# Optimization experiments

Hardware: AMD Instinct MI355X
Metric: run time of the kernel (lower is better)

Reference implementation:

```python
import jax, jax.numpy as jnp
import numpy as np

EPS = 1e-10
MARGIN = 0.05
DELTA = 0.1
H = W = 512
N = 8388608


def setup_inputs() -> dict:
    key = jax.random.key(0)
    k1, k2, k3, k4 = jax.random.split(key, 4)
    v_input = jax.random.uniform(k1, (3, H, W), dtype=jnp.float32)
    coords = jax.random.randint(k2, (N, 4), 0, W, dtype=jnp.int32)  # x1,y1,x2,y2
    darker = jax.random.randint(k3, (N,), 0, 3, dtype=jnp.int32)
    weights = jax.random.uniform(k4, (N,), dtype=jnp.float32)
    return {"v_input": v_input, "coords": coords, "darker": darker, "weights": weights}


def reference(v_input, coords, darker, weights):
    # v = sum over channels / 3, then affine remap (exactly as torch code)
    v = jnp.sum(v_input, axis=0) / 3.0
    v = (v * 255.0 + 1.0) / 256.0  # [H, W]

    x1, y1, x2, y2 = coords[:, 0], coords[:, 1], coords[:, 2], coords[:, 3]
    r1 = v[y1, x1]
    r2 = v[y2, x2]
    ratio = r1 / (r2 + EPS)
    ratio_inv = r2 / (r1 + EPS)

    b = 1.0 + DELTA + MARGIN
    inv_b = 1.0 / b
    # darker == 1: penalize if ratio > 1/b
    l1 = jnp.where(ratio > inv_b, (ratio - inv_b) + (b - ratio_inv), 0.0)
    # darker == 2: penalize if ratio < b
    l2 = jnp.where(ratio < b, (b - ratio) + (ratio_inv - inv_b), 0.0)
    # darker == 0 (margin <= delta branch): two-sided hinge around [bl, br]
    br = 1.0 + DELTA - MARGIN
    bl = 1.0 / br
    l0 = jnp.where(
        ratio > br,
        (ratio - br) + (bl - ratio_inv),
        jnp.where(ratio < bl, (bl - ratio) + (ratio_inv - br), 0.0),
    )

    per = jnp.where(darker == 1, l1, jnp.where(darker == 2, l2, l0))
    loss = jnp.sum(weights * per) / np.float32(coords.shape[0])
    return loss
```

## Files before the change

kernel.cpp:

```cpp
#include <hip/hip_runtime.h>

#define HW 512
#define NPIX (HW * HW)
#define LDS_PIX 163840
#define THREADS 1024
#define BLOCKS 512
#define NB 4

#define EPS_F  1e-10f
constexpr double B_d  = 1.0 + 0.1 + 0.05;
constexpr double BR_d = 1.0 + 0.1 - 0.05;
#define B_F    ((float)B_d)
#define INVB_F ((float)(1.0 / B_d))
#define BR_F   ((float)BR_d)
#define BL_F   ((float)(1.0 / BR_d))

typedef __attribute__((ext_vector_type(4))) int ivec4;

__global__ void build_v(const float* __restrict__ vin,
                        unsigned char* __restrict__ vq,
                        float* __restrict__ out) {
    int i = blockIdx.x * blockDim.x + threadIdx.x;
    if (i == 0) *out = 0.0f;
    if (i < NPIX) {
        float s = vin[i] + vin[i + NPIX] + vin[i + 2 * NPIX];
        float m = s * (1.0f / 3.0f);
        vq[i] = (unsigned char)__float2int_rn(m * 255.0f);
    }
}

__device__ __forceinline__ float rcp_fast(float x) {
#if __has_builtin(__builtin_amdgcn_rcpf)
    return __builtin_amdgcn_rcpf(x);
#else
    return 1.0f / x;
#endif
}

__device__ __forceinline__ float per_loss(float r1, float r2, int d) {
    float ratio = r1 * rcp_fast(r2 + EPS_F);
    float rinv  = r2 * rcp_fast(r1 + EPS_F);
    float l1 = (ratio > INVB_F) ? (ratio - INVB_F + (B_F - rinv)) : 0.0f;
    float l2 = (ratio < B_F)    ? (B_F - ratio + (rinv - INVB_F)) : 0.0f;
    float l0 = (ratio > BR_F)   ? (ratio - BR_F + (BL_F - rinv))
             : ((ratio < BL_F)  ? (BL_F - ratio + (rinv - BR_F)) : 0.0f);
    return (d == 1) ? l1 : ((d == 2) ? l2 : l0);
}


__device__ __forceinline__ void load_c(ivec4 (&cc)[NB], const ivec4* __restrict__ coords,
                                       int tid, int T, int ofs) {
    #pragma unroll
    for (int k = 0; k < NB; ++k)
        cc[k] = __builtin_nontemporal_load(&coords[tid + (ofs + k) * T]);
}

__device__ __forceinline__ void load_dw(int (&dd)[NB], float (&ww)[NB],
                                        const int* __restrict__ darker,
                                        const float* __restrict__ weights,
                                        int tid, int T, int ofs) {
    #pragma unroll
    for (int k = 0; k < NB; ++k)
        dd[k] = __builtin_nontemporal_load(&darker[tid + (ofs + k) * T]);
    #pragma unroll
    for (int k = 0; k < NB; ++k)
        ww[k] = __builtin_nontemporal_load(&weights[tid + (ofs + k) * T]);
}

__device__ __forceinline__ void gather_issue(const ivec4 (&cc)[NB],
        unsigned (&q1)[NB], unsigned (&q2)[NB],
        const unsigned char* lv, const unsigned char* __restrict__ vq) {
    #pragma unroll
    for (int k = 0; k < NB; ++k) {
        int i1 = cc[k].y * HW + cc[k].x;
        int i2 = cc[k].w * HW + cc[k].z;
        if (i1 < LDS_PIX) q1[k] = lv[i1]; else q1[k] = vq[i1];
        if (i2 < LDS_PIX) q2[k] = lv[i2]; else q2[k] = vq[i2];
    }
}

__device__ __forceinline__ void consume(const unsigned (&q1)[NB], const unsigned (&q2)[NB],
                                        const int (&dd)[NB], const float (&ww)[NB],
                                        float& acc) {
    #pragma unroll
    for (int k = 0; k < NB; ++k) {
        float r1 = (float)(q1[k] + 1) * (1.0f / 256.0f);
        float r2 = (float)(q2[k] + 1) * (1.0f / 256.0f);
        acc += ww[k] * per_loss(r1, r2, dd[k]);
    }
}

#define SBAR() __builtin_amdgcn_sched_barrier(0)

__global__ __launch_bounds__(THREADS)
__attribute__((amdgpu_waves_per_eu(4, 4)))
void whdr_kernel(
        const unsigned char* __restrict__ vq,
        const ivec4* __restrict__ coords,
        const int*   __restrict__ darker,
        const float* __restrict__ weights,
        float*       __restrict__ out,
        int n) {
    __shared__ unsigned char lv[LDS_PIX];
    const int tid = blockIdx.x * THREADS + threadIdx.x;
    const int T   = BLOCKS * THREADS;
    float acc = 0.0f;

    if (n == T * NB * 4) {
        ivec4 cA[NB], cB[NB];
        int   dA[NB], dB[NB];
        float wA[NB], wB[NB];
        unsigned qa1[NB], qa2[NB], qb1[NB], qb2[NB];

        load_c (cA, coords, tid, T, 0);
        load_dw(dA, wA, darker, weights, tid, T, 0);
        load_c (cB, coords, tid, T, NB);
        load_dw(dB, wB, darker, weights, tid, T, NB);
        {
            const uint4* s4 = (const uint4*)vq;
            uint4* d4 = (uint4*)lv;
            #pragma unroll
            for (int j = threadIdx.x; j < LDS_PIX / 16; j += THREADS) d4[j] = s4[j];
        }
        __syncthreads();

        gather_issue(cA, qa1, qa2, lv, vq);            SBAR();
        gather_issue(cB, qb1, qb2, lv, vq);            SBAR();
        load_c (cA, coords, tid, T, 2 * NB);           SBAR();
        consume(qa1, qa2, dA, wA, acc);
        load_dw(dA, wA, darker, weights, tid, T, 2 * NB); SBAR();
        gather_issue(cA, qa1, qa2, lv, vq);            SBAR();
        load_c (cB, coords, tid, T, 3 * NB);           SBAR();
        consume(qb1, qb2, dB, wB, acc);
        load_dw(dB, wB, darker, weights, tid, T, 3 * NB); SBAR();
        gather_issue(cB, qb1, qb2, lv, vq);            SBAR();
        consume(qa1, qa2, dA, wA, acc);
        consume(qb1, qb2, dB, wB, acc);
    } else {
        {
            const uint4* s4 = (const uint4*)vq;
            uint4* d4 = (uint4*)lv;
            for (int j = threadIdx.x; j < LDS_PIX / 16; j += THREADS) d4[j] = s4[j];
        }
        __syncthreads();
        const int TT = gridDim.x * THREADS;
        for (int i = tid; i < n; i += TT) {
            ivec4 c = coords[i];
            int i1 = c.y * HW + c.x, i2 = c.w * HW + c.z;
            unsigned a = (i1 < LDS_PIX) ? (unsigned)lv[i1] : (unsigned)vq[i1];
            unsigned b = (i2 < LDS_PIX) ? (unsigned)lv[i2] : (unsigned)vq[i2];
            float r1 = (float)(a + 1) * (1.0f / 256.0f);
            float r2 = (float)(b + 1) * (1.0f / 256.0f);
            acc += weights[i] * per_loss(r1, r2, darker[i]);
        }
    }

    #pragma unroll
    for (int off = 32; off > 0; off >>= 1)
        acc += __shfl_down(acc, off, 64);
    __syncthreads();
    float* wsum = (float*)lv;
    int lane = threadIdx.x & 63;
    int wid  = threadIdx.x >> 6;
    if (lane == 0) wsum[wid] = acc;
    __syncthreads();
    if (threadIdx.x == 0) {
        float s = 0.0f;
        #pragma unroll
        for (int i = 0; i < THREADS / 64; ++i) s += wsum[i];
        atomicAdd(out, s / (float)n);
    }
}

extern "C" void kernel_launch(void* const* d_in, const int* in_sizes, int n_in,
                              void* d_out, int out_size, void* d_ws, size_t ws_size,
                              hipStream_t stream) {
    const float* v_input = (const float*)d_in[0];
    const ivec4* coords  = (const ivec4*)d_in[1];
    const int*   darker  = (const int*)d_in[2];
    const float* weights = (const float*)d_in[3];
    float* out = (float*)d_out;
    unsigned char* vq = (unsigned char*)d_ws;
    int n = in_sizes[2];

    build_v<<<(NPIX + 255) / 256, 256, 0, stream>>>(v_input, vq, out);
    whdr_kernel<<<BLOCKS, THREADS, 0, stream>>>(vq, coords, darker, weights, out, n);
}
```

Measured before the change: 246.7 us.

## Drop LDS staging of pixel table and gather directly from global with deeper pipeline

Removes the per-block copy of 160KB of the quantized image into LDS, so every gather now reads the 256KB byte table straight from global memory, where it should stay cache-resident. The launch goes from 512 blocks of 1024 threads to 2048 blocks of 256 threads, with 8 waves per EU and a macro-unrolled 8-round double-buffered pipeline of 2 elements per round. The intent is to cut the redundant per-block staging traffic and the sync, and to raise occupancy. In exchange, every gather becomes a global/L2 byte load instead of an LDS hit, which adds latency.

```diff
diff --git a/kernel.cpp b/kernel.cpp
--- a/kernel.cpp
+++ b/kernel.cpp
@@ -2,10 +2,10 @@
 
 #define HW 512
 #define NPIX (HW * HW)
-#define LDS_PIX 163840
-#define THREADS 1024
-#define BLOCKS 512
-#define NB 4
+#define THREADS 256
+#define BLOCKS 2048
+#define NB 2
+#define RNDS 8
 
 #define EPS_F  1e-10f
 constexpr double B_d  = 1.0 + 0.1 + 0.05;
@@ -69,13 +69,11 @@
 
 __device__ __forceinline__ void gather_issue(const ivec4 (&cc)[NB],
         unsigned (&q1)[NB], unsigned (&q2)[NB],
-        const unsigned char* lv, const unsigned char* __restrict__ vq) {
+        const unsigned char* __restrict__ vq) {
     #pragma unroll
     for (int k = 0; k < NB; ++k) {
-        int i1 = cc[k].y * HW + cc[k].x;
-        int i2 = cc[k].w * HW + cc[k].z;
-        if (i1 < LDS_PIX) q1[k] = lv[i1]; else q1[k] = vq[i1];
-        if (i2 < LDS_PIX) q2[k] = lv[i2]; else q2[k] = vq[i2];
+        q1[k] = vq[cc[k].y * HW + cc[k].x];
+        q2[k] = vq[cc[k].w * HW + cc[k].z];
     }
 }
 
@@ -93,7 +91,7 @@
 #define SBAR() __builtin_amdgcn_sched_barrier(0)
 
 __global__ __launch_bounds__(THREADS)
-__attribute__((amdgpu_waves_per_eu(4, 4)))
+__attribute__((amdgpu_waves_per_eu(8, 8)))
 void whdr_kernel(
         const unsigned char* __restrict__ vq,
         const ivec4* __restrict__ coords,
@@ -101,54 +99,44 @@
         const float* __restrict__ weights,
         float*       __restrict__ out,
         int n) {
-    __shared__ unsigned char lv[LDS_PIX];
     const int tid = blockIdx.x * THREADS + threadIdx.x;
     const int T   = BLOCKS * THREADS;
     float acc = 0.0f;
 
-    if (n == T * NB * 4) {
+    if (n == T * NB * RNDS) {
         ivec4 cA[NB], cB[NB];
         int   dA[NB], dB[NB];
         float wA[NB], wB[NB];
-        unsigned qa1[NB], qa2[NB], qb1[NB], qb2[NB];
+        unsigned qA1[NB], qA2[NB], qB1[NB], qB2[NB];
 
         load_c (cA, coords, tid, T, 0);
         load_dw(dA, wA, darker, weights, tid, T, 0);
         load_c (cB, coords, tid, T, NB);
         load_dw(dB, wB, darker, weights, tid, T, NB);
-        {
-            const uint4* s4 = (const uint4*)vq;
-            uint4* d4 = (uint4*)lv;
-            #pragma unroll
-            for (int j = threadIdx.x; j < LDS_PIX / 16; j += THREADS) d4[j] = s4[j];
-        }
-        __syncthreads();
+        gather_issue(cA, qA1, qA2, vq);                SBAR();
 
-        gather_issue(cA, qa1, qa2, lv, vq);            SBAR();
-        gather_issue(cB, qb1, qb2, lv, vq);            SBAR();
-        load_c (cA, coords, tid, T, 2 * NB);           SBAR();
-        consume(qa1, qa2, dA, wA, acc);
-        load_dw(dA, wA, darker, weights, tid, T, 2 * NB); SBAR();
-        gather_issue(cA, qa1, qa2, lv, vq);            SBAR();
-        load_c (cB, coords, tid, T, 3 * NB);           SBAR();
-        consume(qb1, qb2, dB, wB, acc);
-        load_dw(dB, wB, darker, weights, tid, T, 3 * NB); SBAR();
-        gather_issue(cB, qb1, qb2, lv, vq);            SBAR();
-        consume(qa1, qa2, dA, wA, acc);
-        consume(qb1, qb2, dB, wB, acc);
+#define RPF(r, CUR, NXT) \
+        gather_issue(c##NXT, q##NXT##1, q##NXT##2, vq);            SBAR(); \
+        load_c (c##CUR, coords, tid, T, (r + 2) * NB);             SBAR(); \
+        consume(q##CUR##1, q##CUR##2, d##CUR, w##CUR, acc); \
+        load_dw(d##CUR, w##CUR, darker, weights, tid, T, (r + 2) * NB); SBAR();
+
+        RPF(0, A, B)
+        RPF(1, B, A)
+        RPF(2, A, B)
+        RPF(3, B, A)
+        RPF(4, A, B)
+        RPF(5, B, A)
+#undef RPF
+        gather_issue(cB, qB1, qB2, vq);                SBAR();
+        consume(qA1, qA2, dA, wA, acc);
+        consume(qB1, qB2, dB, wB, acc);
     } else {
-        {
-            const uint4* s4 = (const uint4*)vq;
-            uint4* d4 = (uint4*)lv;
-            for (int j = threadIdx.x; j < LDS_PIX / 16; j += THREADS) d4[j] = s4[j];
-        }
-        __syncthreads();
         const int TT = gridDim.x * THREADS;
         for (int i = tid; i < n; i += TT) {
             ivec4 c = coords[i];
-            int i1 = c.y * HW + c.x, i2 = c.w * HW + c.z;
-            unsigned a = (i1 < LDS_PIX) ? (unsigned)lv[i1] : (unsigned)vq[i1];
-            unsigned b = (i2 < LDS_PIX) ? (unsigned)lv[i2] : (unsigned)vq[i2];
+            unsigned a = vq[c.y * HW + c.x];
+            unsigned b = vq[c.w * HW + c.z];
             float r1 = (float)(a + 1) * (1.0f / 256.0f);
             float r2 = (float)(b + 1) * (1.0f / 256.0f);
             acc += weights[i] * per_loss(r1, r2, darker[i]);
@@ -158,8 +146,7 @@
     #pragma unroll
     for (int off = 32; off > 0; off >>= 1)
         acc += __shfl_down(acc, off, 64);
-    __syncthreads();
-    float* wsum = (float*)lv;
+    __shared__ float wsum[THREADS / 64];
     int lane = threadIdx.x & 63;
     int wid  = threadIdx.x >> 6;
     if (lane == 0) wsum[wid] = acc;
```

Measured after the change: 316.8 us. 28.4% more time.

## Halve LDS image slice and deepen software pipeline to eight rounds

Applied to the files above, without the earlier changes.

Cuts the LDS-resident part of the quantized image from 160K to 80K pixels, halves the batch per stage, and turns the hand-written two-round pipeline into a macro-driven eight-round rotation. It also drops the fixed waves-per-EU attribute. With less LDS per block, more blocks or waves can be resident to hide gather and stream latency, but more gathers now go to the L2-backed global copy instead of LDS, and the per-block LDS copy is shorter.

```diff
diff --git a/kernel.cpp b/kernel.cpp
--- a/kernel.cpp
+++ b/kernel.cpp
@@ -2,10 +2,11 @@
 
 #define HW 512
 #define NPIX (HW * HW)
-#define LDS_PIX 163840
+#define LDS_PIX 81920
 #define THREADS 1024
 #define BLOCKS 512
-#define NB 4
+#define NB 2
+#define RNDS 8
 
 #define EPS_F  1e-10f
 constexpr double B_d  = 1.0 + 0.1 + 0.05;
@@ -93,7 +94,6 @@
 #define SBAR() __builtin_amdgcn_sched_barrier(0)
 
 __global__ __launch_bounds__(THREADS)
-__attribute__((amdgpu_waves_per_eu(4, 4)))
 void whdr_kernel(
         const unsigned char* __restrict__ vq,
         const ivec4* __restrict__ coords,
@@ -106,11 +106,11 @@
     const int T   = BLOCKS * THREADS;
     float acc = 0.0f;
 
-    if (n == T * NB * 4) {
+    if (n == T * NB * RNDS) {
         ivec4 cA[NB], cB[NB];
         int   dA[NB], dB[NB];
         float wA[NB], wB[NB];
-        unsigned qa1[NB], qa2[NB], qb1[NB], qb2[NB];
+        unsigned qA1[NB], qA2[NB], qB1[NB], qB2[NB];
 
         load_c (cA, coords, tid, T, 0);
         load_dw(dA, wA, darker, weights, tid, T, 0);
@@ -123,19 +123,24 @@
             for (int j = threadIdx.x; j < LDS_PIX / 16; j += THREADS) d4[j] = s4[j];
         }
         __syncthreads();
+        gather_issue(cA, qA1, qA2, lv, vq);            SBAR();
 
-        gather_issue(cA, qa1, qa2, lv, vq);            SBAR();
-        gather_issue(cB, qb1, qb2, lv, vq);            SBAR();
-        load_c (cA, coords, tid, T, 2 * NB);           SBAR();
-        consume(qa1, qa2, dA, wA, acc);
-        load_dw(dA, wA, darker, weights, tid, T, 2 * NB); SBAR();
-        gather_issue(cA, qa1, qa2, lv, vq);            SBAR();
-        load_c (cB, coords, tid, T, 3 * NB);           SBAR();
-        consume(qb1, qb2, dB, wB, acc);
-        load_dw(dB, wB, darker, weights, tid, T, 3 * NB); SBAR();
-        gather_issue(cB, qb1, qb2, lv, vq);            SBAR();
-        consume(qa1, qa2, dA, wA, acc);
-        consume(qb1, qb2, dB, wB, acc);
+#define RPF(r, CUR, NXT) \
+        gather_issue(c##NXT, q##NXT##1, q##NXT##2, lv, vq);        SBAR(); \
+        load_c (c##CUR, coords, tid, T, (r + 2) * NB);             SBAR(); \
+        consume(q##CUR##1, q##CUR##2, d##CUR, w##CUR, acc); \
+        load_dw(d##CUR, w##CUR, darker, weights, tid, T, (r + 2) * NB); SBAR();
+
+        RPF(0, A, B)
+        RPF(1, B, A)
+        RPF(2, A, B)
+        RPF(3, B, A)
+        RPF(4, A, B)
+        RPF(5, B, A)
+#undef RPF
+        gather_issue(cB, qB1, qB2, lv, vq);            SBAR();
+        consume(qA1, qA2, dA, wA, acc);
+        consume(qB1, qB2, dB, wB, acc);
     } else {
         {
             const uint4* s4 = (const uint4*)vq;
```

Measured after the change: 263.4 us. 6.8% more time.
